# Performance work log

Hardware: AMD Instinct MI355X
Metric: run time of the kernel (lower is better)

## Reference

```python
import jax, jax.numpy as jnp
import numpy as np

N = 50000
E = 1600000
IN_DIM = 256
HID = 128
EPS = 1e-5


def _bn(x, gamma, beta):
    # BatchNorm1d forward in training mode: biased batch stats
    mean = jnp.mean(x, axis=0)
    var = jnp.mean((x - mean) ** 2, axis=0)
    return (x - mean) * jax.lax.rsqrt(var + EPS) * gamma + beta


def _sage(x, edge_index, Wl, bl, Wr):
    # PyG SAGEConv with mean aggregation:
    #   out = lin_l(mean_{j in N(i)} x_j) + lin_r(x_i)
    src, dst = edge_index[0], edge_index[1]
    agg = jax.ops.segment_sum(x[src], dst, num_segments=N)          # [N, H]
    cnt = jax.ops.segment_sum(jnp.ones((src.shape[0],), x.dtype), dst, num_segments=N)
    mean = agg / jnp.maximum(cnt, 1.0)[:, None]
    return mean @ Wl + bl + x @ Wr


def setup_inputs() -> dict:
    key = jax.random.key(0)
    ks = jax.random.split(key, 16)
    s_in = 1.0 / np.sqrt(IN_DIM)
    s_h = 1.0 / np.sqrt(HID)
    return {
        "x": jax.random.normal(ks[0], (N, IN_DIM), jnp.float32),
        "edge_index": jax.random.randint(ks[1], (2, E), 0, N, jnp.int32),
        # input_linear: Linear(IN_DIM, HID) + BN
        "W_in": jax.random.uniform(ks[2], (IN_DIM, HID), jnp.float32, -s_in, s_in),
        "b_in": jax.random.uniform(ks[3], (HID,), jnp.float32, -s_in, s_in),
        "g1": jnp.ones((HID,), jnp.float32), "be1": jnp.zeros((HID,), jnp.float32),
        # hidden_linear: Linear(HID, HID) + BN
        "W_hid": jax.random.uniform(ks[4], (HID, HID), jnp.float32, -s_h, s_h),
        "b_hid": jax.random.uniform(ks[5], (HID,), jnp.float32, -s_h, s_h),
        "g2": jnp.ones((HID,), jnp.float32), "be2": jnp.zeros((HID,), jnp.float32),
        # graph_conv1: SAGEConv(HID, HID) + BN
        "Wl1": jax.random.uniform(ks[6], (HID, HID), jnp.float32, -s_h, s_h),
        "bl1": jax.random.uniform(ks[7], (HID,), jnp.float32, -s_h, s_h),
        "Wr1": jax.random.uniform(ks[8], (HID, HID), jnp.float32, -s_h, s_h),
        "g3": jnp.ones((HID,), jnp.float32), "be3": jnp.zeros((HID,), jnp.float32),
        # graph_conv2: SAGEConv(HID, HID) + BN
        "Wl2": jax.random.uniform(ks[9], (HID, HID), jnp.float32, -s_h, s_h),
        "bl2": jax.random.uniform(ks[10], (HID,), jnp.float32, -s_h, s_h),
        "Wr2": jax.random.uniform(ks[11], (HID, HID), jnp.float32, -s_h, s_h),
        "g4": jnp.ones((HID,), jnp.float32), "be4": jnp.zeros((HID,), jnp.float32),
    }


def reference(x, edge_index, W_in, b_in, g1, be1, W_hid, b_hid, g2, be2,
              Wl1, bl1, Wr1, g3, be3, Wl2, bl2, Wr2, g4, be4):
    feat = jax.nn.relu(_bn(x @ W_in + b_in, g1, be1))
    feat = jax.nn.relu(_bn(feat @ W_hid + b_hid, g2, be2))
    out = _bn(_sage(feat, edge_index, Wl1, bl1, Wr1), g3, be3)
    out = _bn(_sage(out, edge_index, Wl2, bl2, Wr2), g4, be4)
    return (feat, out)
```

## Files before the change

kernel.cpp:

```cpp
#include <hip/hip_runtime.h>
#include <stdint.h>

#define NN 50000
#define EE 1600000
#define IN_DIMC 256
#define HIDC 128
#define EPSC 1e-5f

#define NB 196
#define GA 512
#define CHUNK 3125
#define STILE_SHIFT 13
#define NKEY 2048

typedef unsigned short ushort_t;
typedef __attribute__((ext_vector_type(8))) short short8;
typedef __attribute__((ext_vector_type(4))) float floatx4;

static __device__ inline ushort_t f2bf(float f) {
    unsigned int u = __float_as_uint(f);
    u = u + 0x7fffu + ((u >> 16) & 1u);
    return (ushort_t)(u >> 16);
}
static __device__ inline unsigned int pack2(float a, float b) {
    return (unsigned int)f2bf(a) | ((unsigned int)f2bf(b) << 16);
}
static __device__ inline float bf2f(unsigned int bits16) {
    return __uint_as_float(bits16 << 16);
}

__global__ __launch_bounds__(256) void tcvt_all_kernel(
    const float* __restrict__ W_in, const float* __restrict__ W_hid,
    const float* __restrict__ Wl1, const float* __restrict__ Wr1,
    const float* __restrict__ Wl2, const float* __restrict__ Wr2,
    ushort_t* __restrict__ Wt_in, ushort_t* __restrict__ Wt_hid,
    ushort_t* __restrict__ Wtl1, ushort_t* __restrict__ Wtr1,
    ushort_t* __restrict__ Wtl2, ushort_t* __restrict__ Wtr2)
{
    const int idx = blockIdx.x * 256 + threadIdx.x;
    if (idx < 32768) {
        const int n = idx >> 8;
        const int k = idx & 255;
        Wt_in[idx] = f2bf(W_in[(size_t)k * 128 + n]);
    } else if (idx < 32768 + 5 * 16384) {
        const int r = idx - 32768;
        const int seg = r / 16384;
        const int j = r - seg * 16384;
        const int n = j >> 7;
        const int k = j & 127;
        const float* W; ushort_t* Wt;
        switch (seg) {
            case 0: W = W_hid; Wt = Wt_hid; break;
            case 1: W = Wl1;  Wt = Wtl1;  break;
            case 2: W = Wr1;  Wt = Wtr1;  break;
            case 3: W = Wl2;  Wt = Wtl2;  break;
            default: W = Wr2; Wt = Wtr2;  break;
        }
        Wt[j] = f2bf(W[(size_t)k * 128 + n]);
    }
}

__global__ __launch_bounds__(256) void mfma_gemm_kernel(
    const void* __restrict__ A1, const ushort_t* __restrict__ Wt1, int K1, int a1type,
    const void* __restrict__ A2, const ushort_t* __restrict__ Wt2, int K2,
    const float* __restrict__ bias, float* __restrict__ C, int M,
    const float* __restrict__ preStats, const float* __restrict__ preG,
    const float* __restrict__ preBe, float* __restrict__ outStats)
{
    __shared__ ushort_t Bs[128 * 136];
    __shared__ __align__(16) float aArr[128], bArr[128];
    __shared__ float red_s[4][128], red_q[4][128];

    const int t    = threadIdx.x;
    const int lane = t & 63;
    const int wave = t >> 6;
    const int quad = lane >> 4;
    const int l15  = lane & 15;
    const int row0 = blockIdx.x * 128 + wave * 32;
    const int doAffine = (preStats != nullptr);

    if (doAffine && t < 128) {
        const float invM = 1.0f / (float)M;
        const float mean = preStats[t] * invM;
        float var = preStats[128 + t] * invM - mean * mean;
        if (var < 0.0f) var = 0.0f;
        const float s = preG[t] / sqrtf(var + EPSC);
        aArr[t] = s;
        bArr[t] = preBe[t] - mean * s;
    }
    if (doAffine) __syncthreads();

    floatx4 acc[2][8];
    #pragma unroll
    for (int i = 0; i < 2; i++)
        #pragma unroll
        for (int j = 0; j < 8; j++)
            acc[i][j] = (floatx4){0.0f, 0.0f, 0.0f, 0.0f};

    const int ksq = quad * 8;
    bool firstChunk = true;

    for (int s = 0; s < 2; s++) {
        const void*     A     = s ? A2  : A1;
        const ushort_t* Wt    = s ? Wt2 : Wt1;
        const int       K     = s ? K2  : K1;
        const int       atype = s ? 1   : a1type;
        if (A == nullptr) continue;

        for (int kc = 0; kc < K; kc += 128) {
            if (!firstChunk) __syncthreads();
            firstChunk = false;

            #pragma unroll
            for (int p = 0; p < 8; p++) {
                const int idx = p * 256 + t;
                const int n   = idx >> 4;
                const int c0  = (idx & 15) * 8;
                *(uint4*)(Bs + n * 136 + c0) =
                    *(const uint4*)(Wt + (size_t)n * K + kc + c0);
            }
            __syncthreads();

            short8 afrag[2][4];
            if (atype == 1) {
                const ushort_t* Ab = (const ushort_t*)A;
                #pragma unroll
                for (int mt = 0; mt < 2; mt++) {
                    int gr = row0 + mt * 16 + l15;
                    if (gr > M - 1) gr = M - 1;
                    const size_t base = (size_t)gr * K + kc + ksq;
                    #pragma unroll
                    for (int ks = 0; ks < 4; ks++)
                        afrag[mt][ks] = *(const short8*)(Ab + base + ks * 32);
                }
            } else {
                const float* Af = (const float*)A;
                #pragma unroll
                for (int mt = 0; mt < 2; mt++) {
                    int gr = row0 + mt * 16 + l15;
                    if (gr > M - 1) gr = M - 1;
                    const size_t base = (size_t)gr * K + kc + ksq;
                    #pragma unroll
                    for (int ks = 0; ks < 4; ks++) {
                        float4 v0 = *(const float4*)(Af + base + ks * 32);
                        float4 v1 = *(const float4*)(Af + base + ks * 32 + 4);
                        if (doAffine && s == 0) {
                            const int k0 = ks * 32 + ksq;
                            const float4 sa0 = *(const float4*)(aArr + k0);
                            const float4 sb0 = *(const float4*)(bArr + k0);
                            const float4 sa1 = *(const float4*)(aArr + k0 + 4);
                            const float4 sb1 = *(const float4*)(bArr + k0 + 4);
                            v0.x = fmaxf(sa0.x * v0.x + sb0.x, 0.0f);
                            v0.y = fmaxf(sa0.y * v0.y + sb0.y, 0.0f);
                            v0.z = fmaxf(sa0.z * v0.z + sb0.z, 0.0f);
                            v0.w = fmaxf(sa0.w * v0.w + sb0.w, 0.0f);
                            v1.x = fmaxf(sa1.x * v1.x + sb1.x, 0.0f);
                            v1.y = fmaxf(sa1.y * v1.y + sb1.y, 0.0f);
                            v1.z = fmaxf(sa1.z * v1.z + sb1.z, 0.0f);
                            v1.w = fmaxf(sa1.w * v1.w + sb1.w, 0.0f);
                        }
                        uint4 w;
                        w.x = pack2(v0.x, v0.y);
                        w.y = pack2(v0.z, v0.w);
                        w.z = pack2(v1.x, v1.y);
                        w.w = pack2(v1.z, v1.w);
                        afrag[mt][ks] = __builtin_bit_cast(short8, w);
                    }
                }
            }

            #pragma unroll
            for (int ks = 0; ks < 4; ks++) {
                const int ko = ks * 32 + ksq;
                short8 b[8];
                #pragma unroll
                for (int j = 0; j < 8; j++)
                    b[j] = *(const short8*)(Bs + (j * 16 + l15) * 136 + ko);
                #pragma unroll
                for (int mt = 0; mt < 2; mt++) {
                    #pragma unroll
                    for (int j = 0; j < 8; j++)
                        acc[mt][j] = __builtin_amdgcn_mfma_f32_16x16x32_bf16(
                            afrag[mt][ks], b[j], acc[mt][j], 0, 0, 0);
                }
            }
        }
    }

    float s_[8], q_[8];
    #pragma unroll
    for (int j = 0; j < 8; j++) { s_[j] = 0.0f; q_[j] = 0.0f; }

    #pragma unroll
    for (int j = 0; j < 8; j++) {
        const int col = j * 16 + l15;
        const float bv = bias[col];
        #pragma unroll
        for (int mt = 0; mt < 2; mt++) {
            const int rbase = row0 + mt * 16 + quad * 4;
            #pragma unroll
            for (int reg = 0; reg < 4; reg++) {
                const float val = acc[mt][j][reg] + bv;
                const int r_ = rbase + reg;
                if (r_ < M) {
                    C[(size_t)r_ * HIDC + col] = val;
                    s_[j] += val;
                    q_[j] += val * val;
                }
            }
        }
    }
    #pragma unroll
    for (int j = 0; j < 8; j++) {
        s_[j] += __shfl_xor(s_[j], 16, 64);
        s_[j] += __shfl_xor(s_[j], 32, 64);
        q_[j] += __shfl_xor(q_[j], 16, 64);
        q_[j] += __shfl_xor(q_[j], 32, 64);
    }
    if (quad == 0) {
        #pragma unroll
        for (int j = 0; j < 8; j++) {
            red_s[wave][j * 16 + l15] = s_[j];
            red_q[wave][j * 16 + l15] = q_[j];
        }
    }
    __syncthreads();
    if (t < 128) {
        const float S = red_s[0][t] + red_s[1][t] + red_s[2][t] + red_s[3][t];
        const float Q = red_q[0][t] + red_q[1][t] + red_q[2][t] + red_q[3][t];
        atomicAdd(&outStats[t], S);
        atomicAdd(&outStats[128 + t], Q);
    }
}

__global__ __launch_bounds__(256) void bn_apply_kernel(
    const float* __restrict__ src, float* __restrict__ dstF,
    ushort_t* __restrict__ dstB, const float* __restrict__ stats,
    const float* __restrict__ gamma, const float* __restrict__ beta,
    int relu, int M)
{
    __shared__ float sc[128], sh[128];
    const int t = threadIdx.x;
    if (t < 128) {
        const float invM = 1.0f / (float)M;
        const float mean = stats[t] * invM;
        float var = stats[128 + t] * invM - mean * mean;
        if (var < 0.0f) var = 0.0f;
        const float s = gamma[t] / sqrtf(var + EPSC);
        sc[t] = s;
        sh[t] = beta[t] - mean * s;
    }
    __syncthreads();

    const int total4 = M * HIDC / 4;
    for (int i = blockIdx.x * 256 + t; i < total4; i += gridDim.x * 256) {
        float4 v = ((const float4*)src)[i];
        const int c = (i * 4) & 127;
        v.x = v.x * sc[c]     + sh[c];
        v.y = v.y * sc[c + 1] + sh[c + 1];
        v.z = v.z * sc[c + 2] + sh[c + 2];
        v.w = v.w * sc[c + 3] + sh[c + 3];
        if (relu) {
            v.x = fmaxf(v.x, 0.0f); v.y = fmaxf(v.y, 0.0f);
            v.z = fmaxf(v.z, 0.0f); v.w = fmaxf(v.w, 0.0f);
        }
        if (dstF) ((float4*)dstF)[i] = v;
        if (dstB) {
            uint2 w;
            w.x = pack2(v.x, v.y);
            w.y = pack2(v.z, v.w);
            *(uint2*)(dstB + (size_t)i * 4) = w;
        }
    }
}

__global__ __launch_bounds__(256) void bucket_hist_kernel(
    const int* __restrict__ dstArr, int* __restrict__ hist2D)
{
    __shared__ int hist[NB];
    const int t = threadIdx.x;
    for (int i = t; i < NB; i += 256) hist[i] = 0;
    __syncthreads();
    const int e0 = blockIdx.x * CHUNK;
    const int e1 = e0 + CHUNK;
    for (int e = e0 + t; e < e1; e += 256)
        atomicAdd(&hist[dstArr[e] >> 8], 1);
    __syncthreads();
    for (int i = t; i < NB; i += 256)
        hist2D[(size_t)i * GA + blockIdx.x] = hist[i];
}

__global__ __launch_bounds__(256) void bucket_offsets_kernel(
    int* __restrict__ hist2D, int* __restrict__ bucketBase, int* __restrict__ rowp)
{
    __shared__ int wtot[4];
    const int t = threadIdx.x;
    int tot = 0;
    if (t < NB) {
        int4* p = (int4*)(hist2D + (size_t)t * GA);
        int s = 0;
        for (int i = 0; i < GA / 4; i++) {
            int4 h = p[i];
            int4 o;
            o.x = s; s += h.x;
            o.y = s; s += h.y;
            o.z = s; s += h.z;
            o.w = s; s += h.w;
            p[i] = o;
        }
        tot = s;
    }
    const int lane = t & 63, w = t >> 6;
    int x = tot;
    #pragma unroll
    for (int off = 1; off < 64; off <<= 1) {
        const int y = __shfl_up(x, off);
        if (lane >= off) x += y;
    }
    if (lane == 63) wtot[w] = x;
    __syncthreads();
    int woff = 0;
    #pragma unroll
    for (int j = 0; j < 4; j++) if (j < w) woff += wtot[j];
    const int excl = x + woff - tot;
    if (t < NB) bucketBase[t] = excl;
    if (t == 0) { bucketBase[NB] = EE; rowp[NN] = EE; }
}

__global__ __launch_bounds__(256) void bucket_scatter_kernel(
    const int* __restrict__ srcArr, const int* __restrict__ dstArr,
    const int* __restrict__ hist2D, const int* __restrict__ bucketBase,
    int2* __restrict__ ebuf)
{
    __shared__ int cur[NB];
    const int t = threadIdx.x;
    for (int i = t; i < NB; i += 256)
        cur[i] = bucketBase[i] + hist2D[(size_t)i * GA + blockIdx.x];
    __syncthreads();
    const int e0 = blockIdx.x * CHUNK;
    const int e1 = e0 + CHUNK;
    for (int e = e0 + t; e < e1; e += 256) {
        const int d = dstArr[e];
        const int s = srcArr[e];
        const int p = atomicAdd(&cur[d >> 8], 1);
        ebuf[p] = make_int2(s, d);
    }
}

__global__ __launch_bounds__(256) void fine_sort_kernel(
    const int2* __restrict__ ebuf, const int* __restrict__ bucketBase,
    int* __restrict__ rowp, int* __restrict__ col)
{
    __shared__ int cnt[NKEY];
    __shared__ int wtot[4];
    const int b = blockIdx.x;
    const int t = threadIdx.x;
    const int bb0 = bucketBase[b];
    const int bb1 = bucketBase[b + 1];
    #pragma unroll
    for (int i = 0; i < 8; i++) cnt[t * 8 + i] = 0;
    __syncthreads();
    for (int e = bb0 + t; e < bb1; e += 256) {
        const int2 sd = ebuf[e];
        const int key = ((sd.y & 255) << 3) | (sd.x >> STILE_SHIFT);
        atomicAdd(&cnt[key], 1);
    }
    __syncthreads();
    int loc[8];
    int tot = 0;
    #pragma unroll
    for (int i = 0; i < 8; i++) { loc[i] = tot; tot += cnt[t * 8 + i]; }
    const int lane = t & 63, w = t >> 6;
    int x = tot;
    #pragma unroll
    for (int off = 1; off < 64; off <<= 1) {
        const int y = __shfl_up(x, off);
        if (lane >= off) x += y;
    }
    if (lane == 63) wtot[w] = x;
    __syncthreads();
    int woff = 0;
    #pragma unroll
    for (int j = 0; j < 4; j++) if (j < w) woff += wtot[j];
    const int excl = x + woff - tot;
    const int node = b * 256 + t;
    if (node < NN) rowp[node] = bb0 + excl;
    __syncthreads();
    #pragma unroll
    for (int i = 0; i < 8; i++) cnt[t * 8 + i] = excl + loc[i];
    __syncthreads();
    for (int e = bb0 + t; e < bb1; e += 256) {
        const int2 sd = ebuf[e];
        const int key = ((sd.y & 255) << 3) | (sd.x >> STILE_SHIFT);
        const int p = atomicAdd(&cnt[key], 1);
        col[bb0 + p] = sd.x;
    }
}

__global__ __launch_bounds__(256) void agg_kernel(
    const ushort_t* __restrict__ F, const int* __restrict__ row_ptr,
    const int* __restrict__ col, ushort_t* __restrict__ Mout)
{
    const int lane = threadIdx.x & 63;
    const int wave = blockIdx.x * (blockDim.x >> 6) + (threadIdx.x >> 6);
    const int nwaves = gridDim.x * (blockDim.x >> 6);
    const int coff = lane * 2;

    for (int n = wave; n < NN; n += nwaves) {
        const int b = __builtin_amdgcn_readfirstlane(row_ptr[n]);
        const int e = __builtin_amdgcn_readfirstlane(row_ptr[n + 1]);
        const int deg = e - b;
        float accx = 0.0f, accy = 0.0f;
        int j = b;
        for (; j + 8 <= e; j += 8) {
            const int s0 = col[j + 0];
            const int s1 = col[j + 1];
            const int s2 = col[j + 2];
            const int s3 = col[j + 3];
            const int s4 = col[j + 4];
            const int s5 = col[j + 5];
            const int s6 = col[j + 6];
            const int s7 = col[j + 7];
            const unsigned int v0 = *(const unsigned int*)(F + (size_t)s0 * HIDC + coff);
            const unsigned int v1 = *(const unsigned int*)(F + (size_t)s1 * HIDC + coff);
            const unsigned int v2 = *(const unsigned int*)(F + (size_t)s2 * HIDC + coff);
            const unsigned int v3 = *(const unsigned int*)(F + (size_t)s3 * HIDC + coff);
            const unsigned int v4 = *(const unsigned int*)(F + (size_t)s4 * HIDC + coff);
            const unsigned int v5 = *(const unsigned int*)(F + (size_t)s5 * HIDC + coff);
            const unsigned int v6 = *(const unsigned int*)(F + (size_t)s6 * HIDC + coff);
            const unsigned int v7 = *(const unsigned int*)(F + (size_t)s7 * HIDC + coff);
            accx += bf2f(v0 & 0xffffu) + bf2f(v1 & 0xffffu) + bf2f(v2 & 0xffffu)
                  + bf2f(v3 & 0xffffu) + bf2f(v4 & 0xffffu) + bf2f(v5 & 0xffffu)
                  + bf2f(v6 & 0xffffu) + bf2f(v7 & 0xffffu);
            accy += bf2f(v0 >> 16) + bf2f(v1 >> 16) + bf2f(v2 >> 16)
                  + bf2f(v3 >> 16) + bf2f(v4 >> 16) + bf2f(v5 >> 16)
                  + bf2f(v6 >> 16) + bf2f(v7 >> 16);
        }
        for (; j < e; j++) {
            const int s = col[j];
            const unsigned int v = *(const unsigned int*)(F + (size_t)s * HIDC + coff);
            accx += bf2f(v & 0xffffu);
            accy += bf2f(v >> 16);
        }
        const float inv = 1.0f / (float)(deg > 1 ? deg : 1);
        *(unsigned int*)(Mout + (size_t)n * HIDC + coff) =
            pack2(accx * inv, accy * inv);
    }
}

extern "C" void kernel_launch(void* const* d_in, const int* in_sizes, int n_in,
                              void* d_out, int out_size, void* d_ws, size_t ws_size,
                              hipStream_t stream)
{
    const float* x     = (const float*)d_in[0];
    const int*   ei    = (const int*)  d_in[1];
    const float* W_in  = (const float*)d_in[2];
    const float* b_in  = (const float*)d_in[3];
    const float* g1    = (const float*)d_in[4];
    const float* be1   = (const float*)d_in[5];
    const float* W_hid = (const float*)d_in[6];
    const float* b_hid = (const float*)d_in[7];
    const float* g2    = (const float*)d_in[8];
    const float* be2   = (const float*)d_in[9];
    const float* Wl1   = (const float*)d_in[10];
    const float* bl1   = (const float*)d_in[11];
    const float* Wr1   = (const float*)d_in[12];
    const float* g3    = (const float*)d_in[13];
    const float* be3   = (const float*)d_in[14];
    const float* Wl2   = (const float*)d_in[15];
    const float* bl2   = (const float*)d_in[16];
    const float* Wr2   = (const float*)d_in[17];
    const float* g4    = (const float*)d_in[18];
    const float* be4   = (const float*)d_in[19];

    const int* srcArr = ei;
    const int* dstArr = ei + EE;

    char* ws = (char*)d_ws;
    float*    bufA      = (float*)ws;    ws += (size_t)NN * HIDC * sizeof(float);
    float*    bufB      = (float*)ws;    ws += (size_t)NN * HIDC * sizeof(float);
    ushort_t* featB16   = (ushort_t*)ws; ws += (size_t)NN * HIDC * sizeof(ushort_t);
    ushort_t* o3B16     = (ushort_t*)ws; ws += (size_t)NN * HIDC * sizeof(ushort_t);
    ushort_t* aggB16    = (ushort_t*)ws; ws += (size_t)NN * HIDC * sizeof(ushort_t);
    float*    stats     = (float*)ws;    ws += 4 * 256 * sizeof(float);
    int*      hist2D    = (int*)ws;      ws += (size_t)NB * GA * sizeof(int);
    int*      bucketBase= (int*)ws;      ws += (NB + 4) * sizeof(int);
    int*      rowp      = (int*)ws;      ws += (size_t)(NN + 4) * sizeof(int);
    int*      colIdx    = (int*)ws;      ws += (size_t)EE * sizeof(int);
    int2*     ebuf      = (int2*)ws;     ws += (size_t)EE * sizeof(int2);
    ushort_t* Wt_in     = (ushort_t*)ws; ws += 128 * 256 * sizeof(ushort_t);
    ushort_t* Wt_hid    = (ushort_t*)ws; ws += 128 * 128 * sizeof(ushort_t);
    ushort_t* Wtl1      = (ushort_t*)ws; ws += 128 * 128 * sizeof(ushort_t);
    ushort_t* Wtr1      = (ushort_t*)ws; ws += 128 * 128 * sizeof(ushort_t);
    ushort_t* Wtl2      = (ushort_t*)ws; ws += 128 * 128 * sizeof(ushort_t);
    ushort_t* Wtr2      = (ushort_t*)ws; ws += 128 * 128 * sizeof(ushort_t);

    float* out0 = (float*)d_out;
    float* out1 = out0 + (size_t)NN * HIDC;

    hipMemsetAsync(stats, 0, 4 * 256 * sizeof(float), stream);

    tcvt_all_kernel<<<448, 256, 0, stream>>>(W_in, W_hid, Wl1, Wr1, Wl2, Wr2,
                                             Wt_in, Wt_hid, Wtl1, Wtr1, Wtl2, Wtr2);

    bucket_hist_kernel<<<GA, 256, 0, stream>>>(dstArr, hist2D);
    bucket_offsets_kernel<<<1, 256, 0, stream>>>(hist2D, bucketBase, rowp);
    bucket_scatter_kernel<<<GA, 256, 0, stream>>>(srcArr, dstArr, hist2D,
                                                  bucketBase, ebuf);
    fine_sort_kernel<<<NB, 256, 0, stream>>>(ebuf, bucketBase, rowp, colIdx);

    const int gemmGrid = (NN + 127) / 128;

    mfma_gemm_kernel<<<gemmGrid, 256, 0, stream>>>(
        x, Wt_in, IN_DIMC, 0, nullptr, nullptr, 0,
        b_in, bufA, NN, nullptr, nullptr, nullptr, stats + 0);

    mfma_gemm_kernel<<<gemmGrid, 256, 0, stream>>>(
        bufA, Wt_hid, HIDC, 0, nullptr, nullptr, 0,
        b_hid, bufB, NN, stats + 0, g1, be1, stats + 256);

    bn_apply_kernel<<<1024, 256, 0, stream>>>(bufB, out0, featB16,
                                              stats + 256, g2, be2, 1, NN);

    agg_kernel<<<4096, 256, 0, stream>>>(featB16, rowp, colIdx, aggB16);
    mfma_gemm_kernel<<<gemmGrid, 256, 0, stream>>>(
        aggB16, Wtl1, HIDC, 1, featB16, Wtr1, HIDC,
        bl1, bufA, NN, nullptr, nullptr, nullptr, stats + 512);

    bn_apply_kernel<<<1024, 256, 0, stream>>>(bufA, nullptr, o3B16,
                                              stats + 512, g3, be3, 0, NN);

    agg_kernel<<<4096, 256, 0, stream>>>(o3B16, rowp, colIdx, aggB16);
    mfma_gemm_kernel<<<gemmGrid, 256, 0, stream>>>(
        aggB16, Wtl2, HIDC, 1, o3B16, Wtr2, HIDC,
        bl2, bufB, NN, nullptr, nullptr, nullptr, stats + 768);

    bn_apply_kernel<<<1024, 256, 0, stream>>>(bufB, out1, nullptr,
                                              stats + 768, g4, be4, 0, NN);
}
```

Baseline: 441.5 us.

## Pack edge indices into 16-bit fields and aggregate two nodes per wave

Edges in the sort buffer are packed into one 32-bit word (src in the high 16 bits, dst in the low 16 bits), and column indices are stored as 16-bit values, cutting the bytes moved in scatter, sort and aggregation. The aggregation kernel now has each wave handle exactly two nodes with interleaved 8-edge loads to raise memory-level parallelism, using a fixed grid of 6250 blocks. The packing only holds because N is below 65536, so 16 bits are enough for src and dst.

```diff
diff --git a/kernel.cpp b/kernel.cpp
--- a/kernel.cpp
+++ b/kernel.cpp
@@ -330,7 +330,7 @@
 __global__ __launch_bounds__(256) void bucket_scatter_kernel(
     const int* __restrict__ srcArr, const int* __restrict__ dstArr,
     const int* __restrict__ hist2D, const int* __restrict__ bucketBase,
-    int2* __restrict__ ebuf)
+    unsigned int* __restrict__ ebuf)
 {
     __shared__ int cur[NB];
     const int t = threadIdx.x;
@@ -343,13 +343,13 @@
         const int d = dstArr[e];
         const int s = srcArr[e];
         const int p = atomicAdd(&cur[d >> 8], 1);
-        ebuf[p] = make_int2(s, d);
+        ebuf[p] = ((unsigned int)s << 16) | (unsigned int)d;
     }
 }
 
 __global__ __launch_bounds__(256) void fine_sort_kernel(
-    const int2* __restrict__ ebuf, const int* __restrict__ bucketBase,
-    int* __restrict__ rowp, int* __restrict__ col)
+    const unsigned int* __restrict__ ebuf, const int* __restrict__ bucketBase,
+    int* __restrict__ rowp, ushort_t* __restrict__ col)
 {
     __shared__ int cnt[NKEY];
     __shared__ int wtot[4];
@@ -361,8 +361,8 @@
     for (int i = 0; i < 8; i++) cnt[t * 8 + i] = 0;
     __syncthreads();
     for (int e = bb0 + t; e < bb1; e += 256) {
-        const int2 sd = ebuf[e];
-        const int key = ((sd.y & 255) << 3) | (sd.x >> STILE_SHIFT);
+        const unsigned int sd = ebuf[e];
+        const int key = (int)((sd & 255u) << 3) | (int)(sd >> (16 + STILE_SHIFT));
         atomicAdd(&cnt[key], 1);
     }
     __syncthreads();
@@ -390,62 +390,94 @@
     for (int i = 0; i < 8; i++) cnt[t * 8 + i] = excl + loc[i];
     __syncthreads();
     for (int e = bb0 + t; e < bb1; e += 256) {
-        const int2 sd = ebuf[e];
-        const int key = ((sd.y & 255) << 3) | (sd.x >> STILE_SHIFT);
+        const unsigned int sd = ebuf[e];
+        const int key = (int)((sd & 255u) << 3) | (int)(sd >> (16 + STILE_SHIFT));
         const int p = atomicAdd(&cnt[key], 1);
-        col[bb0 + p] = sd.x;
+        col[bb0 + p] = (ushort_t)(sd >> 16);
     }
 }
 
 __global__ __launch_bounds__(256) void agg_kernel(
     const ushort_t* __restrict__ F, const int* __restrict__ row_ptr,
-    const int* __restrict__ col, ushort_t* __restrict__ Mout)
+    const ushort_t* __restrict__ col, ushort_t* __restrict__ Mout)
 {
     const int lane = threadIdx.x & 63;
-    const int wave = blockIdx.x * (blockDim.x >> 6) + (threadIdx.x >> 6);
-    const int nwaves = gridDim.x * (blockDim.x >> 6);
+    const int wv   = blockIdx.x * 4 + (threadIdx.x >> 6);
+    const int n0   = wv * 2;
+    const int n1   = n0 + 1;
     const int coff = lane * 2;
 
-    for (int n = wave; n < NN; n += nwaves) {
-        const int b = __builtin_amdgcn_readfirstlane(row_ptr[n]);
-        const int e = __builtin_amdgcn_readfirstlane(row_ptr[n + 1]);
-        const int deg = e - b;
-        float accx = 0.0f, accy = 0.0f;
-        int j = b;
-        for (; j + 8 <= e; j += 8) {
-            const int s0 = col[j + 0];
-            const int s1 = col[j + 1];
-            const int s2 = col[j + 2];
-            const int s3 = col[j + 3];
-            const int s4 = col[j + 4];
-            const int s5 = col[j + 5];
-            const int s6 = col[j + 6];
-            const int s7 = col[j + 7];
-            const unsigned int v0 = *(const unsigned int*)(F + (size_t)s0 * HIDC + coff);
-            const unsigned int v1 = *(const unsigned int*)(F + (size_t)s1 * HIDC + coff);
-            const unsigned int v2 = *(const unsigned int*)(F + (size_t)s2 * HIDC + coff);
-            const unsigned int v3 = *(const unsigned int*)(F + (size_t)s3 * HIDC + coff);
-            const unsigned int v4 = *(const unsigned int*)(F + (size_t)s4 * HIDC + coff);
-            const unsigned int v5 = *(const unsigned int*)(F + (size_t)s5 * HIDC + coff);
-            const unsigned int v6 = *(const unsigned int*)(F + (size_t)s6 * HIDC + coff);
-            const unsigned int v7 = *(const unsigned int*)(F + (size_t)s7 * HIDC + coff);
-            accx += bf2f(v0 & 0xffffu) + bf2f(v1 & 0xffffu) + bf2f(v2 & 0xffffu)
-                  + bf2f(v3 & 0xffffu) + bf2f(v4 & 0xffffu) + bf2f(v5 & 0xffffu)
-                  + bf2f(v6 & 0xffffu) + bf2f(v7 & 0xffffu);
-            accy += bf2f(v0 >> 16) + bf2f(v1 >> 16) + bf2f(v2 >> 16)
-                  + bf2f(v3 >> 16) + bf2f(v4 >> 16) + bf2f(v5 >> 16)
-                  + bf2f(v6 >> 16) + bf2f(v7 >> 16);
-        }
-        for (; j < e; j++) {
-            const int s = col[j];
-            const unsigned int v = *(const unsigned int*)(F + (size_t)s * HIDC + coff);
-            accx += bf2f(v & 0xffffu);
-            accy += bf2f(v >> 16);
-        }
-        const float inv = 1.0f / (float)(deg > 1 ? deg : 1);
-        *(unsigned int*)(Mout + (size_t)n * HIDC + coff) =
-            pack2(accx * inv, accy * inv);
-    }
+    const int b0 = __builtin_amdgcn_readfirstlane(row_ptr[n0]);
+    const int e0 = __builtin_amdgcn_readfirstlane(row_ptr[n0 + 1]);
+    const int b1 = __builtin_amdgcn_readfirstlane(row_ptr[n1]);
+    const int e1 = __builtin_amdgcn_readfirstlane(row_ptr[n1 + 1]);
+
+    float a0x = 0.0f, a0y = 0.0f, a1x = 0.0f, a1y = 0.0f;
+    int j0 = b0, j1 = b1;
+
+    while (j0 + 8 <= e0 && j1 + 8 <= e1) {
+        int s0[8], s1[8];
+        #pragma unroll
+        for (int i = 0; i < 8; i++) s0[i] = col[j0 + i];
+        #pragma unroll
+        for (int i = 0; i < 8; i++) s1[i] = col[j1 + i];
+        unsigned int v0[8], v1[8];
+        #pragma unroll
+        for (int i = 0; i < 8; i++)
+            v0[i] = *(const unsigned int*)(F + (size_t)s0[i] * HIDC + coff);
+        #pragma unroll
+        for (int i = 0; i < 8; i++)
+            v1[i] = *(const unsigned int*)(F + (size_t)s1[i] * HIDC + coff);
+        #pragma unroll
+        for (int i = 0; i < 8; i++) {
+            a0x += bf2f(v0[i] & 0xffffu); a0y += bf2f(v0[i] >> 16);
+        }
+        #pragma unroll
+        for (int i = 0; i < 8; i++) {
+            a1x += bf2f(v1[i] & 0xffffu); a1y += bf2f(v1[i] >> 16);
+        }
+        j0 += 8; j1 += 8;
+    }
+    for (; j0 + 8 <= e0; j0 += 8) {
+        int s0[8];
+        #pragma unroll
+        for (int i = 0; i < 8; i++) s0[i] = col[j0 + i];
+        unsigned int v0[8];
+        #pragma unroll
+        for (int i = 0; i < 8; i++)
+            v0[i] = *(const unsigned int*)(F + (size_t)s0[i] * HIDC + coff);
+        #pragma unroll
+        for (int i = 0; i < 8; i++) {
+            a0x += bf2f(v0[i] & 0xffffu); a0y += bf2f(v0[i] >> 16);
+        }
+    }
+    for (; j1 + 8 <= e1; j1 += 8) {
+        int s1[8];
+        #pragma unroll
+        for (int i = 0; i < 8; i++) s1[i] = col[j1 + i];
+        unsigned int v1[8];
+        #pragma unroll
+        for (int i = 0; i < 8; i++)
+            v1[i] = *(const unsigned int*)(F + (size_t)s1[i] * HIDC + coff);
+        #pragma unroll
+        for (int i = 0; i < 8; i++) {
+            a1x += bf2f(v1[i] & 0xffffu); a1y += bf2f(v1[i] >> 16);
+        }
+    }
+    for (; j0 < e0; j0++) {
+        const unsigned int v = *(const unsigned int*)(F + (size_t)col[j0] * HIDC + coff);
+        a0x += bf2f(v & 0xffffu); a0y += bf2f(v >> 16);
+    }
+    for (; j1 < e1; j1++) {
+        const unsigned int v = *(const unsigned int*)(F + (size_t)col[j1] * HIDC + coff);
+        a1x += bf2f(v & 0xffffu); a1y += bf2f(v >> 16);
+    }
+
+    const int d0 = e0 - b0, d1 = e1 - b1;
+    const float i0 = 1.0f / (float)(d0 > 1 ? d0 : 1);
+    const float i1 = 1.0f / (float)(d1 > 1 ? d1 : 1);
+    *(unsigned int*)(Mout + (size_t)n0 * HIDC + coff) = pack2(a0x * i0, a0y * i0);
+    *(unsigned int*)(Mout + (size_t)n1 * HIDC + coff) = pack2(a1x * i1, a1y * i1);
 }
 
 extern "C" void kernel_launch(void* const* d_in, const int* in_sizes, int n_in,
@@ -486,8 +518,8 @@
     int*      hist2D    = (int*)ws;      ws += (size_t)NB * GA * sizeof(int);
     int*      bucketBase= (int*)ws;      ws += (NB + 4) * sizeof(int);
     int*      rowp      = (int*)ws;      ws += (size_t)(NN + 4) * sizeof(int);
-    int*      colIdx    = (int*)ws;      ws += (size_t)EE * sizeof(int);
-    int2*     ebuf      = (int2*)ws;     ws += (size_t)EE * sizeof(int2);
+    ushort_t* colIdx    = (ushort_t*)ws; ws += (size_t)EE * sizeof(ushort_t) + 64;
+    unsigned int* ebuf  = (unsigned int*)ws; ws += (size_t)EE * sizeof(unsigned int);
     ushort_t* Wt_in     = (ushort_t*)ws; ws += 128 * 256 * sizeof(ushort_t);
     ushort_t* Wt_hid    = (ushort_t*)ws; ws += 128 * 128 * sizeof(ushort_t);
     ushort_t* Wtl1      = (ushort_t*)ws; ws += 128 * 128 * sizeof(ushort_t);
@@ -522,7 +554,7 @@
     bn_apply_kernel<<<1024, 256, 0, stream>>>(bufB, out0, featB16,
                                               stats + 256, g2, be2, 1, NN);
 
-    agg_kernel<<<4096, 256, 0, stream>>>(featB16, rowp, colIdx, aggB16);
+    agg_kernel<<<6250, 256, 0, stream>>>(featB16, rowp, colIdx, aggB16);
     mfma_gemm_kernel<<<gemmGrid, 256, 0, stream>>>(
         aggB16, Wtl1, HIDC, 1, featB16, Wtr1, HIDC,
         bl1, bufA, NN, nullptr, nullptr, nullptr, stats + 512);
@@ -530,7 +562,7 @@
     bn_apply_kernel<<<1024, 256, 0, stream>>>(bufA, nullptr, o3B16,
                                               stats + 512, g3, be3, 0, NN);
 
-    agg_kernel<<<4096, 256, 0, stream>>>(o3B16, rowp, colIdx, aggB16);
+    agg_kernel<<<6250, 256, 0, stream>>>(o3B16, rowp, colIdx, aggB16);
     mfma_gemm_kernel<<<gemmGrid, 256, 0, stream>>>(
         aggB16, Wtl2, HIDC, 1, o3B16, Wtr2, HIDC,
         bl2, bufB, NN, nullptr, nullptr, nullptr, stats + 768);
```

After: 444.6 us. Within noise of the previous version (+0.7%).
